# Kernel tuning notes

Measured on AMD Instinct MI355X. Metric: run time of the kernel, lower is better.

Reference implementation:

```python
import jax, jax.numpy as jnp
import numpy as np

G = 160          # voxel grid extent per axis
N = 300000       # active voxels
CIN, COUT = 64, 128
EPS = 1e-4       # BatchNorm eps from module (0.0001)


def _neighbor_table(pos):
    """pos: [N,3] int32 in [0,G). Returns idx [27,N] int32, -1 where no neighbor voxel exists."""
    n = pos.shape[0]
    flat = (pos[:, 0] * G + pos[:, 1]) * G + pos[:, 2]
    grid = jnp.full((G * G * G,), -1, dtype=jnp.int32).at[flat].set(
        jnp.arange(n, dtype=jnp.int32))
    offs = jnp.array([[dx, dy, dz] for dx in (-1, 0, 1)
                      for dy in (-1, 0, 1) for dz in (-1, 0, 1)], dtype=jnp.int32)
    npos = pos[None, :, :] + offs[:, None, :]              # [27,N,3]
    inb = jnp.all((npos >= 0) & (npos < G), axis=-1)       # [27,N]
    nflat = (npos[..., 0] * G + npos[..., 1]) * G + npos[..., 2]
    nflat = jnp.where(inb, nflat, 0)
    return jnp.where(inb, grid[nflat], -1)                 # [27,N]


def _sparse_conv(feat, nbr_idx, W):
    """Submanifold sparse 3x3x3 conv. feat [N,Cin], nbr_idx [27,N], W [27,Cin,Cout]."""
    n = feat.shape[0]
    acc0 = jnp.zeros((n, W.shape[-1]), dtype=feat.dtype)

    def body(acc, xs):
        idx, Wk = xs                                       # [N], [Cin,Cout]
        valid = (idx >= 0)
        g = feat[jnp.maximum(idx, 0)] * valid[:, None].astype(feat.dtype)
        return acc + g @ Wk, None

    out, _ = jax.lax.scan(body, acc0, (nbr_idx, W))
    return out


def _bn(x, gamma, beta, mean, var):
    # eval-mode BatchNorm1d: (x - mean) / sqrt(var + eps) * gamma + beta
    return (x - mean) * jax.lax.rsqrt(var + EPS) * gamma + beta


def setup_inputs() -> dict:
    key = jax.random.key(0)
    ks = jax.random.split(key, 8)
    rng = np.random.default_rng(0)
    flat = rng.choice(G * G * G, size=N, replace=False)
    pos = np.stack(np.unravel_index(flat, (G, G, G)), axis=-1).astype(np.int32)

    feat = jax.random.normal(ks[0], (N, CIN), dtype=jnp.float32)
    lin_w = jax.random.normal(ks[1], (COUT, CIN), dtype=jnp.float32) / np.sqrt(CIN)
    W1 = jax.random.normal(ks[2], (27, CIN, COUT), dtype=jnp.float32) / np.sqrt(27 * CIN)
    W2 = jax.random.normal(ks[3], (27, COUT, COUT), dtype=jnp.float32) / np.sqrt(27 * COUT)
    return {
        "feat": feat,
        "pos": jnp.asarray(pos),
        "lin_w": lin_w,
        "bn1_gamma": jnp.ones((CIN,), jnp.float32),
        "bn1_beta": jnp.zeros((CIN,), jnp.float32),
        "bn1_mean": 0.1 * jax.random.normal(ks[4], (CIN,), dtype=jnp.float32),
        "bn1_var": 0.5 + jax.random.uniform(ks[5], (CIN,), dtype=jnp.float32),
        "W1": W1,
        "bn2_gamma": jnp.ones((COUT,), jnp.float32),
        "bn2_beta": jnp.zeros((COUT,), jnp.float32),
        "bn2_mean": 0.1 * jax.random.normal(ks[6], (COUT,), dtype=jnp.float32),
        "bn2_var": 0.5 + jax.random.uniform(ks[7], (COUT,), dtype=jnp.float32),
        "W2": W2,
    }


def reference(feat, pos, lin_w, bn1_gamma, bn1_beta, bn1_mean, bn1_var, W1,
              bn2_gamma, bn2_beta, bn2_mean, bn2_var, W2):
    nbr_idx = _neighbor_table(pos)                     # [27,N]
    out1 = feat @ lin_w.T                              # NetworkInNetwork skip
    h = jnp.maximum(_bn(feat, bn1_gamma, bn1_beta, bn1_mean, bn1_var), 0.0)  # LeakyReLU(0)==ReLU
    h = _sparse_conv(h, nbr_idx, W1)
    h = jnp.maximum(_bn(h, bn2_gamma, bn2_beta, bn2_mean, bn2_var), 0.0)
    h = _sparse_conv(h, nbr_idx, W2)
    return out1 + h
```

## Files before the change

kernel.cpp:

```cpp
#include <hip/hip_runtime.h>

#define G    160
#define G3   (G*G*G)
#define NV   300000
#define EPS  1e-4f
#define CAP  24576
#define CPAD 32
#define PCAP 655360
#define TOTIDX 896
#define NS1  (27*192)
#define GGB  2048

typedef unsigned short u16;
typedef __attribute__((ext_vector_type(8))) short bf16x8;
typedef __attribute__((ext_vector_type(4))) float f32x4;

#define OFF_PART 0ull
#define OFF_GRID 0ull
#define OFF_PIN  167772160ull
#define OFF_PDST (OFF_PIN  + 2654208ull)
#define OFF_RI   (OFF_PDST + 2654208ull)
#define OFF_CNT  (OFF_RI   + 1200000ull)
#define OFF_H0   (OFF_CNT  + 8192ull)
#define OFF_H1   (OFF_H0   + 38400000ull)
#define OFF_S2   (OFF_H1   + 76800000ull)
#define OFF_W1T  (OFF_S2   + 76800000ull)
#define OFF_W2T  (OFF_W1T  + 442368ull)
#define OFF_LINW (OFF_W2T  + 884736ull)
#define OFF_BNP  (OFF_LINW + 16384ull)
#define WS_NEED  (OFF_BNP  + 1024ull)

__device__ __forceinline__ u16 f2bf(float f) {
  unsigned u = __float_as_uint(f);
  return (u16)((u + 0x7fffu + ((u >> 16) & 1u)) >> 16);
}
__device__ __forceinline__ float bf2f(u16 h) {
  return __uint_as_float(((unsigned)h) << 16);
}

__global__ __launch_bounds__(256) void k_pairs(const int* __restrict__ pos,
                        const int* __restrict__ grid,
                        int* __restrict__ pin, int* __restrict__ pdst,
                        int* __restrict__ rowinfo, int* __restrict__ counts) {
  __shared__ int lcnt[27];
  __shared__ int wboff[27][4];
  __shared__ int gbase[27];
  __shared__ int scan[256];
  __shared__ int sgb;
  int t = threadIdx.x, lane = t & 63, wv = t >> 6;
  if (t < 27) lcnt[t] = 0;
  int i = blockIdx.x * 256 + t;
  bool act = (i < NV);
  int p0 = 0, p1 = 1 << 20, p2 = 0;
  if (act) { p0 = pos[3*i]; p1 = pos[3*i+1]; p2 = pos[3*i+2]; }
  __syncthreads();

  int j[26];
  #pragma unroll
  for (int kk = 0; kk < 26; kk++) {
    int k = kk < 13 ? kk : kk + 1;
    int q0 = p0 + k/9 - 1, q1 = p1 + (k/3)%3 - 1, q2 = p2 + k%3 - 1;
    bool inb = (q0 >= 0 && q0 < G && q1 >= 0 && q1 < G && q2 >= 0 && q2 < G);
    int addr = inb ? (q0*G + q1)*G + q2 : 0;
    int jj = grid[addr];
    j[kk] = inb ? jj : -1;
  }

  unsigned vmask = 0;
  #pragma unroll
  for (int kk = 0; kk < 26; kk++) if (j[kk] >= 0) vmask |= 1u << kk;
  int ci = __popc(vmask);

  unsigned long long m[26];
  #pragma unroll
  for (int kk = 0; kk < 26; kk++) m[kk] = __ballot(j[kk] >= 0);

  #pragma unroll
  for (int kk = 0; kk < 26; kk++) {
    int k = kk < 13 ? kk : kk + 1;
    if (lane == 0) wboff[k][wv] = atomicAdd(&lcnt[k], (int)__popcll(m[kk]));
  }
  scan[t] = ci;
  __syncthreads();
  #pragma unroll
  for (int d = 1; d < 256; d <<= 1) {
    int val = (t >= d) ? scan[t - d] : 0;
    __syncthreads();
    scan[t] += val;
    __syncthreads();
  }
  if (t < 27 && t != 13)
    gbase[t] = atomicAdd(&counts[t * CPAD], lcnt[t]);
  if (t == 255) sgb = atomicAdd(&counts[TOTIDX], scan[255]);
  __syncthreads();

  int rbase = sgb + scan[t] - ci;
  int cw = (rbase + ci > PCAP) ? 0 : ci;
  if (act) rowinfo[i] = (rbase << 5) | cw;

  #pragma unroll
  for (int kk = 0; kk < 26; kk++) {
    if (j[kk] >= 0) {
      int k = kk < 13 ? kk : kk + 1;
      int slot = gbase[k] + wboff[k][wv] + (int)__popcll(m[kk] & ((1ull << lane) - 1ull));
      int dst = rbase + __popc(vmask & ((1u << kk) - 1u));
      if (slot < CAP) {
        pin[k*CAP + slot]  = j[kk];
        pdst[k*CAP + slot] = (dst < PCAP) ? dst : -1;
      }
    }
  }
}

#define NB_BN   18750
#define NB_GRID 1172
__global__ __launch_bounds__(256) void k_prep(const float* __restrict__ feat,
                          const int* __restrict__ pos, int* __restrict__ grid,
                          const float* __restrict__ g1, const float* __restrict__ b1,
                          const float* __restrict__ m1, const float* __restrict__ v1,
                          u16* __restrict__ h0,
                          const float* __restrict__ W1, const float* __restrict__ W2,
                          const float* __restrict__ linw,
                          const float* __restrict__ g2, const float* __restrict__ b2,
                          const float* __restrict__ m2, const float* __restrict__ v2,
                          u16* __restrict__ w1t, u16* __restrict__ w2t,
                          u16* __restrict__ lwt, float* __restrict__ bnp) {
  __shared__ float shf[8192];
  int b = blockIdx.x, t = threadIdx.x;
  if (b < NB_BN) {
    float* ss = shf; float* tt = shf + 64;
    if (t < 64) { float s = g1[t] * rsqrtf(v1[t] + EPS); ss[t] = s; tt[t] = b1[t] - m1[t]*s; }
    __syncthreads();
    long gt = (long)b * 256 + t;
    int c = (int)(gt & 15) * 4;
    float4 x = ((const float4*)feat)[gt];
    ushort4 q;
    q.x = f2bf(fmaxf(x.x*ss[c  ] + tt[c  ], 0.f));
    q.y = f2bf(fmaxf(x.y*ss[c+1] + tt[c+1], 0.f));
    q.z = f2bf(fmaxf(x.z*ss[c+2] + tt[c+2], 0.f));
    q.w = f2bf(fmaxf(x.w*ss[c+3] + tt[c+3], 0.f));
    ((ushort4*)h0)[gt] = q;
  } else if (b < NB_BN + NB_GRID) {
    int i = (b - NB_BN) * 256 + t;
    if (i < NV)
      grid[(pos[3*i] * G + pos[3*i+1]) * G + pos[3*i+2]] = i;
  } else {
    int bb = b - NB_BN - NB_GRID;
    float* tmp = shf;
    if (bb < 27) {
      const float* src = W1 + bb * 8192;
      u16* dst = w1t + bb * 8192;
      for (int u = t; u < 8192; u += 256) tmp[u] = src[u];
      __syncthreads();
      for (int u = t; u < 8192; u += 256) { int c = u >> 6, a = u & 63; dst[c*64 + a] = f2bf(tmp[a*128 + c]); }
    } else if (bb < 54) {
      int k = bb - 27;
      const float* src = W2 + k * 16384;
      u16* dst = w2t + k * 16384;
      for (int h = 0; h < 2; h++) {
        for (int u = t; u < 8192; u += 256) tmp[u] = src[h*8192 + u];
        __syncthreads();
        for (int u = t; u < 8192; u += 256) { int c = u >> 6, a = u & 63; dst[c*128 + h*64 + a] = f2bf(tmp[a*128 + c]); }
        __syncthreads();
      }
    } else if (bb == 54) {
      for (int u = t; u < 8192; u += 256) lwt[u] = f2bf(linw[u]);
    } else {
      if (t < 128) { float s = g2[t] * rsqrtf(v2[t] + EPS); bnp[t] = s; bnp[128 + t] = b2[t] - m2[t]*s; }
    }
  }
}

template<int K, int RS>
__device__ __forceinline__ void stage_rows(const u16* __restrict__ src, const int* sidx, u16* lds) {
  const int LPR = K / 8, RPI = 256 / LPR;
  int t = threadIdx.x, o = t % LPR, r0 = t / LPR;
  #pragma unroll
  for (int r = r0; r < 128; r += RPI) {
    int j = sidx[r];
    int4 val = make_int4(0, 0, 0, 0);
    if (j >= 0) val = *(const int4*)(src + (long)j * RS + o * 8);
    *(int4*)(lds + r * (K + 8) + o * 8) = val;
  }
}

__device__ __forceinline__ void stage_feat(const float* __restrict__ feat, int row0, u16* lds) {
  int t = threadIdx.x, o = t & 15, r0 = t >> 4;
  #pragma unroll
  for (int r = r0; r < 128; r += 16) {
    int row = row0 + r;
    float4 x = make_float4(0.f, 0.f, 0.f, 0.f);
    if (row < NV) x = *(const float4*)(feat + (long)row * 64 + o * 4);
    ushort4 q; q.x = f2bf(x.x); q.y = f2bf(x.y); q.z = f2bf(x.z); q.w = f2bf(x.w);
    *(ushort4*)(lds + r * 72 + o * 4) = q;
  }
}

template<int K>
__device__ __forceinline__ void mma_tile(const u16* As, const u16* __restrict__ wt, f32x4 acc[4][4]) {
  int lane = threadIdx.x & 63, wave = threadIdx.x >> 6;
  int wr = (wave >> 1) * 64, wc = (wave & 1) * 64;
  int lr = lane & 15, lk = (lane >> 4) * 8;
  #pragma unroll
  for (int kk = 0; kk < K; kk += 32) {
    bf16x8 a[4], b[4];
    #pragma unroll
    for (int f = 0; f < 4; f++) a[f] = *(const bf16x8*)(As + (wr + f*16 + lr) * (K + 8) + kk + lk);
    #pragma unroll
    for (int f = 0; f < 4; f++) b[f] = *(const bf16x8*)(wt + (wc + f*16 + lr) * K + kk + lk);
    #pragma unroll
    for (int fr = 0; fr < 4; fr++)
      #pragma unroll
      for (int fc = 0; fc < 4; fc++)
        acc[fr][fc] = __builtin_amdgcn_mfma_f32_16x16x32_bf16(a[fr], b[fc], acc[fr][fc], 0, 0, 0);
  }
}

__device__ __forceinline__ void spill_acc(const f32x4 acc[4][4], u16* As) {
  int t = threadIdx.x, lane = t & 63, wave = t >> 6;
  int wr = (wave >> 1) * 64, wc = (wave & 1) * 64, cr = (lane >> 4) * 4, cc = lane & 15;
  #pragma unroll
  for (int fr = 0; fr < 4; fr++)
    #pragma unroll
    for (int r = 0; r < 4; r++)
      #pragma unroll
      for (int fc = 0; fc < 4; fc++)
        As[(wr + fr*16 + cr + r) * 136 + wc + fc*16 + cc] = f2bf(acc[fr][fc][r]);
}

__global__ __launch_bounds__(256, 4) void k_c1(const u16* __restrict__ h0,
                                               const u16* __restrict__ w1t,
                                               const int* __restrict__ pin,
                                               const int* __restrict__ pdst,
                                               const int* __restrict__ counts,
                                               u16* __restrict__ partial,
                                               u16* __restrict__ h1) {
  __shared__ __align__(16) u16 As[128 * 136];
  __shared__ int sin[128], sdst[128];
  int bx = blockIdx.x, t = threadIdx.x;
  if (bx < NS1) {
    int k = bx / 192, base = (bx % 192) * 128;
    int cnt = counts[k * CPAD]; if (cnt > CAP) cnt = CAP;
    if (base >= cnt) return;
    if (t < 128) sin[t] = (base + t < cnt) ? pin[k*CAP + base + t] : -1;
    else         sdst[t - 128] = (base + t - 128 < cnt) ? pdst[k*CAP + base + t - 128] : -1;
    __syncthreads();
    stage_rows<64, 64>(h0, sin, As);
    __syncthreads();
    f32x4 acc[4][4] = {};
    mma_tile<64>(As, w1t + k * 8192, acc);
    __syncthreads();
    spill_acc(acc, As);
    __syncthreads();
    #pragma unroll
    for (int u = t; u < 2048; u += 256) {
      int r = u >> 4, o = u & 15;
      int d = sdst[r];
      if (d >= 0)
        *(int4*)(partial + (long)d * 128 + o * 8) = *(const int4*)(As + r * 136 + o * 8);
    }
  } else {
    int row0 = (bx - NS1) * 128;
    if (t < 128) sin[t] = (row0 + t < NV) ? row0 + t : -1;
    __syncthreads();
    stage_rows<64, 64>(h0, sin, As);
    __syncthreads();
    f32x4 acc[4][4] = {};
    mma_tile<64>(As, w1t + 13 * 8192, acc);
    __syncthreads();
    spill_acc(acc, As);
    __syncthreads();
    #pragma unroll
    for (int u = t; u < 2048; u += 256) {
      int r = u >> 4, o = u & 15;
      if (row0 + r < NV)
        *(int4*)(h1 + (long)(row0 + r) * 128 + o * 8) = *(const int4*)(As + r * 136 + o * 8);
    }
  }
}

__global__ __launch_bounds__(256, 4) void k_c2(const float* __restrict__ feat,
                                               const u16* __restrict__ lwt,
                                               const u16* __restrict__ h1,
                                               const u16* __restrict__ w2t,
                                               const int* __restrict__ pin,
                                               const int* __restrict__ pdst,
                                               const int* __restrict__ counts,
                                               u16* __restrict__ partial,
                                               u16* __restrict__ s2buf) {
  __shared__ __align__(16) u16 As[128 * 136];
  __shared__ int sin[128], sdst[128];
  int bx = blockIdx.x, t = threadIdx.x;
  if (bx < NS1) {
    int k = bx / 192, base = (bx % 192) * 128;
    int cnt = counts[k * CPAD]; if (cnt > CAP) cnt = CAP;
    if (base >= cnt) return;
    if (t < 128) sin[t] = (base + t < cnt) ? pin[k*CAP + base + t] : -1;
    else         sdst[t - 128] = (base + t - 128 < cnt) ? pdst[k*CAP + base + t - 128] : -1;
    __syncthreads();
    stage_rows<128, 128>(h1, sin, As);
    __syncthreads();
    f32x4 acc[4][4] = {};
    mma_tile<128>(As, w2t + k * 16384, acc);
    __syncthreads();
    spill_acc(acc, As);
    __syncthreads();
    #pragma unroll
    for (int u = t; u < 2048; u += 256) {
      int r = u >> 4, o = u & 15;
      int d = sdst[r];
      if (d >= 0)
        *(int4*)(partial + (long)d * 128 + o * 8) = *(const int4*)(As + r * 136 + o * 8);
    }
  } else {
    int row0 = (bx - NS1) * 128;
    if (t < 128) sin[t] = (row0 + t < NV) ? row0 + t : -1;
    __syncthreads();
    f32x4 acc[4][4] = {};
    stage_feat(feat, row0, As);
    __syncthreads();
    mma_tile<64>(As, lwt, acc);
    __syncthreads();
    stage_rows<128, 128>(h1, sin, As);
    __syncthreads();
    mma_tile<128>(As, w2t + 13 * 16384, acc);
    __syncthreads();
    spill_acc(acc, As);
    __syncthreads();
    #pragma unroll
    for (int u = t; u < 2048; u += 256) {
      int r = u >> 4, o = u & 15;
      if (row0 + r < NV)
        *(int4*)(s2buf + (long)(row0 + r) * 128 + o * 8) = *(const int4*)(As + r * 136 + o * 8);
    }
  }
}


__global__ __launch_bounds__(256) void k_gather1(const int* __restrict__ rowinfo,
                                                 const u16* __restrict__ partial,
                                                 const float* __restrict__ bnp,
                                                 u16* __restrict__ h1) {
  int lane = threadIdx.x & 63;
  int wid  = blockIdx.x * 4 + (threadIdx.x >> 6);
  int stride = gridDim.x * 4;
  float s0 = bnp[lane*2], s1 = bnp[lane*2 + 1];
  float t0 = bnp[128 + lane*2], t1 = bnp[128 + lane*2 + 1];
  int row = wid;
  if (row >= NV) return;
  int ri = rowinfo[row];
  int nrow = row + stride;
  int ri_n = (nrow < NV) ? rowinfo[nrow] : 0;
  int base = (int)((unsigned)ri >> 5), cnt = ri & 31;
  unsigned sv = *(const unsigned*)(h1 + (long)row * 128 + lane*2);
  const u16* pr = partial + (long)base * 128 + lane*2;
  unsigned p0 = 0, p1 = 0;
  if (cnt > 0) p0 = *(const unsigned*)pr;
  if (cnt > 1) p1 = *(const unsigned*)(pr + 128);
  while (true) {
    int nbase = 0, ncnt = 0;
    unsigned nsv = 0, np0 = 0, np1 = 0;
    const u16* npr = partial;
    if (nrow < NV) {
      nbase = (int)((unsigned)ri_n >> 5); ncnt = ri_n & 31;
      nsv = *(const unsigned*)(h1 + (long)nrow * 128 + lane*2);
      npr = partial + (long)nbase * 128 + lane*2;
      if (ncnt > 0) np0 = *(const unsigned*)npr;
      if (ncnt > 1) np1 = *(const unsigned*)(npr + 128);
    }
    int nnrow = nrow + stride;
    int ri_nn = (nnrow < NV) ? rowinfo[nnrow] : 0;
    float c0 = bf2f((u16)(sv & 0xffff)) + bf2f((u16)(p0 & 0xffff)) + bf2f((u16)(p1 & 0xffff));
    float c1 = bf2f((u16)(sv >> 16))    + bf2f((u16)(p0 >> 16))    + bf2f((u16)(p1 >> 16));
    const u16* prt = pr + 256;
    for (int p = 2; p + 2 <= cnt; p += 2) {
      unsigned a = *(const unsigned*)prt;
      unsigned b = *(const unsigned*)(prt + 128);
      c0 += bf2f((u16)(a & 0xffff)) + bf2f((u16)(b & 0xffff));
      c1 += bf2f((u16)(a >> 16))    + bf2f((u16)(b >> 16));
      prt += 256;
    }
    if (cnt > 2 && (cnt & 1)) {
      unsigned a = *(const unsigned*)(pr + (long)(cnt - 1) * 128);
      c0 += bf2f((u16)(a & 0xffff));
      c1 += bf2f((u16)(a >> 16));
    }
    float o0 = fmaxf(c0 * s0 + t0, 0.f), o1 = fmaxf(c1 * s1 + t1, 0.f);
    *(unsigned*)(h1 + (long)row * 128 + lane*2) = (unsigned)f2bf(o0) | ((unsigned)f2bf(o1) << 16);
    if (nrow >= NV) break;
    row = nrow; cnt = ncnt; sv = nsv; p0 = np0; p1 = np1; pr = npr;
    nrow = nnrow; ri_n = ri_nn;
  }
}

__global__ __launch_bounds__(256) void k_gather2(const int* __restrict__ rowinfo,
                                                 const u16* __restrict__ partial,
                                                 const u16* __restrict__ s2buf,
                                                 float* __restrict__ out) {
  int lane = threadIdx.x & 63;
  int wid  = blockIdx.x * 4 + (threadIdx.x >> 6);
  int stride = gridDim.x * 4;
  int row = wid;
  if (row >= NV) return;
  int ri = rowinfo[row];
  int nrow = row + stride;
  int ri_n = (nrow < NV) ? rowinfo[nrow] : 0;
  int base = (int)((unsigned)ri >> 5), cnt = ri & 31;
  unsigned sv = *(const unsigned*)(s2buf + (long)row * 128 + lane*2);
  const u16* pr = partial + (long)base * 128 + lane*2;
  unsigned p0 = 0, p1 = 0;
  if (cnt > 0) p0 = *(const unsigned*)pr;
  if (cnt > 1) p1 = *(const unsigned*)(pr + 128);
  while (true) {
    int nbase = 0, ncnt = 0;
    unsigned nsv = 0, np0 = 0, np1 = 0;
    const u16* npr = partial;
    if (nrow < NV) {
      nbase = (int)((unsigned)ri_n >> 5); ncnt = ri_n & 31;
      nsv = *(const unsigned*)(s2buf + (long)nrow * 128 + lane*2);
      npr = partial + (long)nbase * 128 + lane*2;
      if (ncnt > 0) np0 = *(const unsigned*)npr;
      if (ncnt > 1) np1 = *(const unsigned*)(npr + 128);
    }
    int nnrow = nrow + stride;
    int ri_nn = (nnrow < NV) ? rowinfo[nnrow] : 0;
    float c0 = bf2f((u16)(sv & 0xffff)) + bf2f((u16)(p0 & 0xffff)) + bf2f((u16)(p1 & 0xffff));
    float c1 = bf2f((u16)(sv >> 16))    + bf2f((u16)(p0 >> 16))    + bf2f((u16)(p1 >> 16));
    const u16* prt = pr + 256;
    for (int p = 2; p + 2 <= cnt; p += 2) {
      unsigned a = *(const unsigned*)prt;
      unsigned b = *(const unsigned*)(prt + 128);
      c0 += bf2f((u16)(a & 0xffff)) + bf2f((u16)(b & 0xffff));
      c1 += bf2f((u16)(a >> 16))    + bf2f((u16)(b >> 16));
      prt += 256;
    }
    if (cnt > 2 && (cnt & 1)) {
      unsigned a = *(const unsigned*)(pr + (long)(cnt - 1) * 128);
      c0 += bf2f((u16)(a & 0xffff));
      c1 += bf2f((u16)(a >> 16));
    }
    *(float2*)(out + (long)row * 128 + lane*2) = make_float2(c0, c1);
    if (nrow >= NV) break;
    row = nrow; cnt = ncnt; sv = nsv; p0 = np0; p1 = np1; pr = npr;
    nrow = nnrow; ri_n = ri_nn;
  }
}

extern "C" void kernel_launch(void* const* d_in, const int* in_sizes, int n_in,
                              void* d_out, int out_size, void* d_ws, size_t ws_size,
                              hipStream_t stream) {
  const float* feat = (const float*)d_in[0];
  const int*   pos  = (const int*)d_in[1];
  const float* linw = (const float*)d_in[2];
  const float* g1 = (const float*)d_in[3], *b1 = (const float*)d_in[4];
  const float* m1 = (const float*)d_in[5], *v1 = (const float*)d_in[6];
  const float* W1 = (const float*)d_in[7];
  const float* g2 = (const float*)d_in[8], *b2 = (const float*)d_in[9];
  const float* m2 = (const float*)d_in[10], *v2 = (const float*)d_in[11];
  const float* W2 = (const float*)d_in[12];

  if (ws_size < WS_NEED) return;

  char* ws = (char*)d_ws;
  u16*   partial = (u16*)(ws + OFF_PART);
  int*   grid    = (int*)(ws + OFF_GRID);
  int*   pin     = (int*)(ws + OFF_PIN);
  int*   pdst    = (int*)(ws + OFF_PDST);
  int*   rowinfo = (int*)(ws + OFF_RI);
  int*   counts  = (int*)(ws + OFF_CNT);
  u16*   h0      = (u16*)(ws + OFF_H0);
  u16*   h1      = (u16*)(ws + OFF_H1);
  u16*   s2buf   = (u16*)(ws + OFF_S2);
  u16*   w1t     = (u16*)(ws + OFF_W1T);
  u16*   w2t     = (u16*)(ws + OFF_W2T);
  u16*   lwt     = (u16*)(ws + OFF_LINW);
  float* bnp     = (float*)(ws + OFF_BNP);
  float* out     = (float*)d_out;

  hipMemsetAsync(grid,  0xFF, (size_t)G3 * 4, stream);
  hipMemsetAsync(counts, 0, 8192, stream);

  k_prep <<<NB_BN + NB_GRID + 56, 256, 0, stream>>>(feat, pos, grid, g1, b1, m1, v1, h0,
                                                    W1, W2, linw, g2, b2, m2, v2,
                                                    w1t, w2t, lwt, bnp);
  k_pairs<<<(NV + 255) / 256, 256, 0, stream>>>(pos, grid, pin, pdst, rowinfo, counts);

  int nself = (NV + 127) / 128;
  k_c1     <<<NS1 + nself, 256, 0, stream>>>(h0, w1t, pin, pdst, counts, partial, h1);
  k_gather1<<<GGB, 256, 0, stream>>>(rowinfo, partial, bnp, h1);
  k_c2     <<<NS1 + nself, 256, 0, stream>>>(feat, lwt, h1, w2t, pin, pdst, counts, partial, s2buf);
  k_gather2<<<GGB, 256, 0, stream>>>(rowinfo, partial, s2buf, out);
}
```

Measured before the change: 627.1 us.

## Split conv2 K dimension into halves to overlap gather staging with MFMA

```diff
diff --git a/kernel.cpp b/kernel.cpp
--- a/kernel.cpp
+++ b/kernel.cpp
@@ -10,6 +10,7 @@
 #define TOTIDX 896
 #define NS1  (27*192)
 #define GGB  2048
+#define HSZ  9216
 
 typedef unsigned short u16;
 typedef __attribute__((ext_vector_type(8))) short bf16x8;
@@ -184,6 +185,18 @@
   }
 }
 
+__device__ __forceinline__ void stage_half(const u16* __restrict__ src, const int* sidx,
+                                           u16* lds, int koff) {
+  int t = threadIdx.x, o = t & 7, r0 = t >> 3;
+  #pragma unroll
+  for (int r = r0; r < 128; r += 32) {
+    int j = sidx[r];
+    int4 val = make_int4(0, 0, 0, 0);
+    if (j >= 0) val = *(const int4*)(src + (long)j * 128 + koff + o * 8);
+    *(int4*)(lds + r * 72 + o * 8) = val;
+  }
+}
+
 __device__ __forceinline__ void stage_feat(const float* __restrict__ feat, int row0, u16* lds) {
   int t = threadIdx.x, o = t & 15, r0 = t >> 4;
   #pragma unroll
@@ -208,6 +221,26 @@
     for (int f = 0; f < 4; f++) a[f] = *(const bf16x8*)(As + (wr + f*16 + lr) * (K + 8) + kk + lk);
     #pragma unroll
     for (int f = 0; f < 4; f++) b[f] = *(const bf16x8*)(wt + (wc + f*16 + lr) * K + kk + lk);
+    #pragma unroll
+    for (int fr = 0; fr < 4; fr++)
+      #pragma unroll
+      for (int fc = 0; fc < 4; fc++)
+        acc[fr][fc] = __builtin_amdgcn_mfma_f32_16x16x32_bf16(a[fr], b[fc], acc[fr][fc], 0, 0, 0);
+  }
+}
+
+__device__ __forceinline__ void mma_half(const u16* As, const u16* __restrict__ wt, int koff,
+                                         f32x4 acc[4][4]) {
+  int lane = threadIdx.x & 63, wave = threadIdx.x >> 6;
+  int wr = (wave >> 1) * 64, wc = (wave & 1) * 64;
+  int lr = lane & 15, lk = (lane >> 4) * 8;
+  #pragma unroll
+  for (int kk = 0; kk < 64; kk += 32) {
+    bf16x8 a[4], b[4];
+    #pragma unroll
+    for (int f = 0; f < 4; f++) a[f] = *(const bf16x8*)(As + (wr + f*16 + lr) * 72 + kk + lk);
+    #pragma unroll
+    for (int f = 0; f < 4; f++) b[f] = *(const bf16x8*)(wt + (wc + f*16 + lr) * 128 + koff + kk + lk);
     #pragma unroll
     for (int fr = 0; fr < 4; fr++)
       #pragma unroll
@@ -288,7 +321,7 @@
                                                const int* __restrict__ counts,
                                                u16* __restrict__ partial,
                                                u16* __restrict__ s2buf) {
-  __shared__ __align__(16) u16 As[128 * 136];
+  __shared__ __align__(16) u16 As[128 * 144];
   __shared__ int sin[128], sdst[128];
   int bx = blockIdx.x, t = threadIdx.x;
   if (bx < NS1) {
@@ -298,10 +331,13 @@
     if (t < 128) sin[t] = (base + t < cnt) ? pin[k*CAP + base + t] : -1;
     else         sdst[t - 128] = (base + t - 128 < cnt) ? pdst[k*CAP + base + t - 128] : -1;
     __syncthreads();
-    stage_rows<128, 128>(h1, sin, As);
+    stage_half(h1, sin, As, 0);
     __syncthreads();
     f32x4 acc[4][4] = {};
-    mma_tile<128>(As, w2t + k * 16384, acc);
+    stage_half(h1, sin, As + HSZ, 64);
+    mma_half(As, w2t + k * 16384, 0, acc);
+    __syncthreads();
+    mma_half(As + HSZ, w2t + k * 16384, 64, acc);
     __syncthreads();
     spill_acc(acc, As);
     __syncthreads();
@@ -319,11 +355,13 @@
     f32x4 acc[4][4] = {};
     stage_feat(feat, row0, As);
     __syncthreads();
+    stage_half(h1, sin, As + HSZ, 0);
     mma_tile<64>(As, lwt, acc);
     __syncthreads();
-    stage_rows<128, 128>(h1, sin, As);
-    __syncthreads();
-    mma_tile<128>(As, w2t + 13 * 16384, acc);
+    stage_half(h1, sin, As, 64);
+    mma_half(As + HSZ, w2t + 13 * 16384, 0, acc);
+    __syncthreads();
+    mma_half(As, w2t + 13 * 16384, 64, acc);
     __syncthreads();
     spill_acc(acc, As);
     __syncthreads();
```

After: 633.0 us. About the same (+1.0%).
